# Optimization experiments

Measured on AMD Instinct MI355X. Metric: run time of the kernel, lower is better.

## Reference

```python
import jax, jax.numpy as jnp
import numpy as np

N, S, E, H = 2, 2048, 1024, 16
D = E // H  # head_dim = 64


def setup_inputs() -> dict:
    key = jax.random.key(0)
    k1, k2, k3 = jax.random.split(key, 3)
    x = jax.random.normal(k1, (N, S, E), dtype=jnp.float32)
    # Xavier-uniform-scaled weights (torch Linear layout: [out_features, in_features])
    lim_qkv = (6.0 / (E + 3 * E)) ** 0.5
    qkv_w = jax.random.uniform(k2, (3 * E, E), dtype=jnp.float32, minval=-lim_qkv, maxval=lim_qkv)
    lim_o = (6.0 / (E + E)) ** 0.5
    o_w = jax.random.uniform(k3, (E, E), dtype=jnp.float32, minval=-lim_o, maxval=lim_o)
    # causal look-ahead mask: positions where mask == 0 are excluded
    attn_mask = jnp.tril(jnp.ones((S, S), dtype=jnp.int32))
    return {"x": x, "attn_mask": attn_mask, "qkv_w": qkv_w, "o_w": o_w}


def reference(x, attn_mask, qkv_w, o_w):
    n, s, e = x.shape
    qkv = x @ qkv_w.T                              # (N, S, 3E)
    q, k, v = jnp.split(qkv, 3, axis=-1)
    # (N, S, E) -> (N, H, S, D)
    def to_heads(t):
        return t.reshape(n, s, H, D).transpose(0, 2, 1, 3)
    q, k, v = to_heads(q), to_heads(k), to_heads(v)
    scale = 1.0 / jnp.sqrt(jnp.asarray(D, dtype=x.dtype))
    logits = jnp.einsum('bhqd,bhkd->bhqk', q, k) * scale   # (N, H, S, S)
    mask = attn_mask.reshape(1, 1, s, s)                    # expand_mask: 2D -> (1,1,S,S)
    logits = jnp.where(mask == 0, -jnp.inf, logits)
    attn_weights = jax.nn.softmax(logits, axis=-1)
    values = jnp.einsum('bhqk,bhkd->bhqd', attn_weights, v)  # (N, H, S, D)
    values = values.transpose(0, 2, 1, 3).reshape(n, s, e)
    o = values @ o_w.T
    return o
```

## Files before the change

kernel.cpp:

```cpp
#include <hip/hip_runtime.h>
#include <math.h>

typedef unsigned short u16;
typedef unsigned int uint;
typedef __attribute__((ext_vector_type(8))) short bf16x8;
typedef __attribute__((ext_vector_type(8))) _Float16 half8;
typedef __attribute__((ext_vector_type(4))) float floatx4;

__device__ __forceinline__ u16 f2bf(float f) {
  union { float f; uint u; } c; c.f = f;
  return (u16)((c.u + 0x7FFFu + ((c.u >> 16) & 1u)) >> 16);
}
__device__ __forceinline__ float bf2f(u16 h) {
  union { uint u; float f; } c; c.u = ((uint)h) << 16;
  return c.f;
}
__device__ __forceinline__ u16 h2u(_Float16 h) {
  union { _Float16 h; u16 u; } c; c.h = h;
  return c.u;
}

#if __has_builtin(__builtin_amdgcn_exp2f)
#define EX2 __builtin_amdgcn_exp2f
#else
#define EX2 exp2f
#endif

__device__ __forceinline__ void gl_lds16(const u16* g, u16* l) {
  __builtin_amdgcn_global_load_lds(
      (const __attribute__((address_space(1))) uint*)g,
      (__attribute__((address_space(3))) uint*)l, 16, 0, 0);
}

__device__ __forceinline__ void store_c(u16* p, float v) { *p = f2bf(v); }
__device__ __forceinline__ void store_c(float* p, float v) { *p = v; }

#define ROR16(x, n)                                                        \
  __builtin_bit_cast(float, __builtin_amdgcn_update_dpp(                   \
      __builtin_bit_cast(int, (x)), __builtin_bit_cast(int, (x)),          \
      0x120 + (n), 0xF, 0xF, false))
__device__ __forceinline__ float rsum16(float x) {
  x += ROR16(x, 8); x += ROR16(x, 4); x += ROR16(x, 2); x += ROR16(x, 1);
  return x;
}

__global__ __launch_bounds__(256) void cvt_all(const float* __restrict__ x,
                                               const float* __restrict__ qw,
                                               const float* __restrict__ ow,
                                               u16* __restrict__ xb,
                                               u16* __restrict__ wb,
                                               u16* __restrict__ ob) {
  int bx = blockIdx.x;
  const float* src; u16* dst; int off;
  if (bx < 2048) { src = x; dst = xb; off = bx; }
  else if (bx < 3584) { src = qw; dst = wb; off = bx - 2048; }
  else { src = ow; dst = ob; off = bx - 3584; }
  int i = (off * 256 + threadIdx.x) * 8;
  float4 a = *(const float4*)(src + i);
  float4 b = *(const float4*)(src + i + 4);
  bf16x8 r;
  r[0] = (short)f2bf(a.x); r[1] = (short)f2bf(a.y);
  r[2] = (short)f2bf(a.z); r[3] = (short)f2bf(a.w);
  r[4] = (short)f2bf(b.x); r[5] = (short)f2bf(b.y);
  r[6] = (short)f2bf(b.z); r[7] = (short)f2bf(b.w);
  *(bf16x8*)(dst + i) = r;
}

__global__ __launch_bounds__(256) void vtrans(const u16* __restrict__ qkv,
                                              u16* __restrict__ vt) {
  constexpr int S = 2048, E = 1024, TE = 3072;
  __shared__ u16 tile[64 * 72];
  const int t = threadIdx.x;
  const int kv0 = blockIdx.x * 64;
  const int bh = blockIdx.y, b = bh >> 4, h = bh & 15;
  const u16* src = qkv + (size_t)b * S * TE + 2 * E + h * 64;
#pragma unroll
  for (int i = 0; i < 2; ++i) {
    int c = t + i * 256;
    int kv = c >> 3, d0 = (c & 7) * 8;
    *(bf16x8*)&tile[kv * 72 + d0] = *(const bf16x8*)&src[(size_t)(kv0 + kv) * TE + d0];
  }
  __syncthreads();
  u16* dst = vt + (size_t)bh * 64 * S + kv0;
#pragma unroll
  for (int i = 0; i < 2; ++i) {
    int c = t + i * 256;
    int d = c >> 3, k0 = (c & 7) * 8;
    bf16x8 r;
#pragma unroll
    for (int j = 0; j < 8; ++j)
      r[j] = (short)h2u((_Float16)bf2f(tile[(k0 + j) * 72 + d]));
    *(bf16x8*)&dst[(size_t)d * S + k0] = r;
  }
}

template <typename TC>
__global__ __launch_bounds__(256) void gemm_bt(const u16* __restrict__ A,
                                               const u16* __restrict__ B,
                                               TC* __restrict__ C,
                                               int K, int N) {
  __shared__ __align__(16) u16 lds_a[128 * 64];
  __shared__ __align__(16) u16 lds_b[128 * 64];
  const int t = threadIdx.x;
  const int w = t >> 6, lane = t & 63, quad = lane >> 4, lr = lane & 15;
  const int wr = w >> 1, wc = w & 1;
  const int m0 = blockIdx.y * 128, n0 = blockIdx.x * 128;

  const int srow = lane >> 3;
  const int scol = ((lane & 7) ^ srow) * 8;
  const u16* Ab = A + (size_t)(m0 + w * 32 + srow) * K + scol;
  const u16* Bb = B + (size_t)(n0 + w * 32 + srow) * K + scol;
  u16* la = lds_a + (w * 32) * 64;
  u16* lb = lds_b + (w * 32) * 64;

  floatx4 acc[4][4];
#pragma unroll
  for (int i = 0; i < 4; ++i)
#pragma unroll
    for (int j = 0; j < 4; ++j) acc[i][j] = {0.f, 0.f, 0.f, 0.f};

  for (int k0 = 0; k0 < K; k0 += 64) {
#pragma unroll
    for (int j = 0; j < 4; ++j) {
      gl_lds16(Ab + (size_t)(j * 8) * K + k0, la + j * 8 * 64);
      gl_lds16(Bb + (size_t)(j * 8) * K + k0, lb + j * 8 * 64);
    }
    __syncthreads();
#pragma unroll
    for (int kk = 0; kk < 2; ++kk) {
      bf16x8 af[4], bfr[4];
#pragma unroll
      for (int mi = 0; mi < 4; ++mi)
        af[mi] = *(const bf16x8*)&lds_a[(wr * 64 + mi * 16 + lr) * 64 +
                                        (((kk * 4 + quad) ^ (lr & 7)) * 8)];
#pragma unroll
      for (int ni = 0; ni < 4; ++ni)
        bfr[ni] = *(const bf16x8*)&lds_b[(wc * 64 + ni * 16 + lr) * 64 +
                                         (((kk * 4 + quad) ^ (lr & 7)) * 8)];
#pragma unroll
      for (int mi = 0; mi < 4; ++mi)
#pragma unroll
        for (int ni = 0; ni < 4; ++ni)
          acc[mi][ni] = __builtin_amdgcn_mfma_f32_16x16x32_bf16(
              af[mi], bfr[ni], acc[mi][ni], 0, 0, 0);
    }
    __syncthreads();
  }
#pragma unroll
  for (int mi = 0; mi < 4; ++mi)
#pragma unroll
    for (int r = 0; r < 4; ++r) {
      int m = m0 + wr * 64 + mi * 16 + quad * 4 + r;
#pragma unroll
      for (int ni = 0; ni < 4; ++ni) {
        int n = n0 + wc * 64 + ni * 16 + lr;
        store_c(&C[(size_t)m * N + n], acc[mi][ni][r]);
      }
    }
}

template <typename TC>
__global__ __launch_bounds__(256) void gemm_bt64(const u16* __restrict__ A,
                                                 const u16* __restrict__ B,
                                                 TC* __restrict__ C,
                                                 int K, int N) {
  __shared__ __align__(16) u16 lds_a[64 * 64];
  __shared__ __align__(16) u16 lds_b[128 * 64];
  const int t = threadIdx.x;
  const int w = t >> 6, lane = t & 63, quad = lane >> 4, lr = lane & 15;
  const int m0 = blockIdx.y * 64, n0 = blockIdx.x * 128;

  const int srow = lane >> 3;
  const int scol = ((lane & 7) ^ srow) * 8;
  const u16* Ab = A + (size_t)(m0 + srow) * K + scol;
  const u16* Bb = B + (size_t)(n0 + srow) * K + scol;

  floatx4 acc[4][2];
#pragma unroll
  for (int i = 0; i < 4; ++i)
#pragma unroll
    for (int j = 0; j < 2; ++j) acc[i][j] = {0.f, 0.f, 0.f, 0.f};

  for (int k0 = 0; k0 < K; k0 += 64) {
#pragma unroll
    for (int i = 0; i < 2; ++i)
      gl_lds16(Ab + (size_t)((w * 2 + i) * 8) * K + k0, &lds_a[(w * 2 + i) * 8 * 64]);
#pragma unroll
    for (int i = 0; i < 4; ++i)
      gl_lds16(Bb + (size_t)((w * 4 + i) * 8) * K + k0, &lds_b[(w * 4 + i) * 8 * 64]);
    __syncthreads();
#pragma unroll
    for (int kk = 0; kk < 2; ++kk) {
      bf16x8 af[4], bfr[2];
#pragma unroll
      for (int mi = 0; mi < 4; ++mi)
        af[mi] = *(const bf16x8*)&lds_a[(mi * 16 + lr) * 64 +
                                        (((kk * 4 + quad) ^ (lr & 7)) * 8)];
#pragma unroll
      for (int ni = 0; ni < 2; ++ni)
        bfr[ni] = *(const bf16x8*)&lds_b[(w * 32 + ni * 16 + lr) * 64 +
                                         (((kk * 4 + quad) ^ (lr & 7)) * 8)];
#pragma unroll
      for (int mi = 0; mi < 4; ++mi)
#pragma unroll
        for (int ni = 0; ni < 2; ++ni)
          acc[mi][ni] = __builtin_amdgcn_mfma_f32_16x16x32_bf16(
              af[mi], bfr[ni], acc[mi][ni], 0, 0, 0);
    }
    __syncthreads();
  }
#pragma unroll
  for (int mi = 0; mi < 4; ++mi)
#pragma unroll
    for (int r = 0; r < 4; ++r) {
      int m = m0 + mi * 16 + quad * 4 + r;
#pragma unroll
      for (int ni = 0; ni < 2; ++ni) {
        int n = n0 + w * 32 + ni * 16 + lr;
        store_c(&C[(size_t)m * N + n], acc[mi][ni][r]);
      }
    }
}

__global__ __launch_bounds__(256, 1) void attn_fwd(const u16* __restrict__ qkv,
                                                   const u16* __restrict__ vt,
                                                   u16* __restrict__ out) {
  constexpr int S = 2048, E = 1024, TE = 3072;
  constexpr float NEG = -1e30f;
  __shared__ __align__(16) u16 lds_k[2][128 * 64];
  __shared__ __align__(16) u16 lds_vt[2][64 * 128];
  __shared__ __align__(16) u16 lds_p[4][16 * 128];
  const int t = threadIdx.x;
  const int w = t >> 6, lane = t & 63, quad = lane >> 4, lr = lane & 15;
  const int lin = (int)blockIdx.x;
  const int xcd = lin & 7, j = lin >> 3;
  const int pass = j >> 5, k = j & 31;
  const int bh = xcd + 8 * (k & 3);
  const int qrank = k >> 2;
  const int qt = pass ? qrank : (15 - qrank);
  const int b = bh >> 4, h = bh & 15;
  const size_t base = (size_t)b * S * TE;
  const u16* kbase = qkv + base + E + h * 64;
  const u16* vtb = vt + (size_t)bh * 64 * S;

  const int s8 = lane >> 3;
  const int kcol = ((lane & 7) ^ s8) * 8;
  const int vrow = lane >> 4;
  u16* const pb = &lds_p[w][0];

  const int q0 = qt * 128;
  const int nkt = qt + 1;

  const float QS = 0.125f * 1.44269504f;
  bf16x8 qf[2][2];
#pragma unroll
  for (int rg = 0; rg < 2; ++rg)
#pragma unroll
    for (int kk = 0; kk < 2; ++kk) {
      bf16x8 q = *(const bf16x8*)&qkv[base +
          (size_t)(q0 + w * 32 + rg * 16 + lr) * TE + h * 64 + kk * 32 + quad * 8];
#pragma unroll
      for (int jj = 0; jj < 8; ++jj) q[jj] = (short)f2bf(bf2f((u16)q[jj]) * QS);
      qf[rg][kk] = q;
    }

  float lst[2][4];
  floatx4 oacc[2][4];
#pragma unroll
  for (int rg = 0; rg < 2; ++rg)
#pragma unroll
    for (int r = 0; r < 4; ++r) { lst[rg][r] = 0.f; }
#pragma unroll
  for (int rg = 0; rg < 2; ++rg)
#pragma unroll
    for (int di = 0; di < 4; ++di) oacc[rg][di] = {0.f, 0.f, 0.f, 0.f};

#pragma unroll
  for (int i = 0; i < 4; ++i) {
    int p0 = w * 8 + i * 32;
    int kv = ((p0 & 15) + s8) * 8 + (p0 >> 4);
    gl_lds16(kbase + (size_t)kv * TE + kcol, &lds_k[0][p0 * 64]);
  }
#pragma unroll
  for (int i = 0; i < 4; ++i) {
    int d0 = w * 4 + i * 16;
    int d = d0 + vrow;
    int cbg = ((lane & 15) ^ (d & 15)) * 8;
    gl_lds16(vtb + (size_t)d * S + cbg, &lds_vt[0][d0 * 128]);
  }

  for (int kt = 0; kt < nkt; ++kt) {
    const int bi = kt & 1;
    __syncthreads();
    if (kt + 1 < nkt) {
      const int bn = bi ^ 1;
#pragma unroll
      for (int i = 0; i < 4; ++i) {
        int p0 = w * 8 + i * 32;
        int kv = 128 * (kt + 1) + ((p0 & 15) + s8) * 8 + (p0 >> 4);
        gl_lds16(kbase + (size_t)kv * TE + kcol, &lds_k[bn][p0 * 64]);
      }
#pragma unroll
      for (int i = 0; i < 4; ++i) {
        int d0 = w * 4 + i * 16;
        int d = d0 + vrow;
        int cbg = ((lane & 15) ^ (d & 15)) * 8;
        gl_lds16(vtb + (size_t)d * S + 128 * (kt + 1) + cbg,
                 &lds_vt[bn][d0 * 128]);
      }
    }

    floatx4 st[2][8];
#pragma unroll
    for (int rg = 0; rg < 2; ++rg)
#pragma unroll
      for (int ni = 0; ni < 8; ++ni) st[rg][ni] = {-4.f, -4.f, -4.f, -4.f};
#pragma unroll
    for (int kk = 0; kk < 2; ++kk) {
      bf16x8 kb[8];
#pragma unroll
      for (int ni = 0; ni < 8; ++ni)
        kb[ni] = *(const bf16x8*)&lds_k[bi][(ni * 16 + lr) * 64 +
                                           (((kk * 4 + quad) ^ (lr & 7)) * 8)];
#pragma unroll
      for (int rg = 0; rg < 2; ++rg)
#pragma unroll
        for (int ni = 0; ni < 8; ++ni)
          st[rg][ni] = __builtin_amdgcn_mfma_f32_16x16x32_bf16(
              qf[rg][kk], kb[ni], st[rg][ni], 0, 0, 0);
    }

    half8 vb[4][4];
#pragma unroll
    for (int kk = 0; kk < 4; ++kk)
#pragma unroll
      for (int di = 0; di < 4; ++di)
        vb[kk][di] = *(const half8*)&lds_vt[bi][(di * 16 + lr) * 128 +
                                                (((kk * 4 + quad) ^ lr) << 3)];

    const bool diag = (kt == nkt - 1);
#pragma unroll
    for (int rg = 0; rg < 2; ++rg) {
#pragma unroll
      for (int r = 0; r < 4; ++r) {
        const int rw = quad * 4 + r;
        const int rloc = w * 32 + rg * 16 + rw;
        if (diag) {
#pragma unroll
          for (int ni = 0; ni < 8; ++ni)
            if (lr * 8 + ni > rloc) st[rg][ni][r] = NEG;
        }
        float pv[8];
#pragma unroll
        for (int ni = 0; ni < 8; ++ni) pv[ni] = EX2(st[rg][ni][r]);
        lst[rg][r] += ((pv[0] + pv[1]) + (pv[2] + pv[3])) +
                      ((pv[4] + pv[5]) + (pv[6] + pv[7]));
        half8 p8;
#pragma unroll
        for (int ni = 0; ni < 8; ++ni) p8[ni] = (_Float16)pv[ni];
        *(half8*)&pb[rw * 128 + (((lr + rw) & 15) << 3)] = p8;
      }
#pragma unroll
      for (int kk = 0; kk < 4; ++kk) {
        half8 pf = *(const half8*)&pb[lr * 128 +
                                      ((((kk * 4 + quad) + lr) & 15) << 3)];
#pragma unroll
        for (int di = 0; di < 4; ++di)
          oacc[rg][di] = __builtin_amdgcn_mfma_f32_16x16x32_f16(
              pf, vb[kk][di], oacc[rg][di], 0, 0, 0);
      }
    }
  }

#pragma unroll
  for (int rg = 0; rg < 2; ++rg)
#pragma unroll
    for (int r = 0; r < 4; ++r) {
      int sg = q0 + w * 32 + rg * 16 + quad * 4 + r;
      float inv_l = 1.f / rsum16(lst[rg][r]);
#pragma unroll
      for (int di = 0; di < 4; ++di)
        out[((size_t)(b * S + sg)) * E + h * 64 + di * 16 + lr] =
            f2bf(oacc[rg][di][r] * inv_l);
    }
}

extern "C" void kernel_launch(void* const* d_in, const int* in_sizes, int n_in,
                              void* d_out, int out_size, void* d_ws, size_t ws_size,
                              hipStream_t stream) {
  constexpr int NB = 2, S = 2048, E = 1024;
  constexpr int M = NB * S;
  const float* x = (const float*)d_in[0];
  const float* qkv_w = (const float*)d_in[2];
  const float* o_w = (const float*)d_in[3];
  float* out = (float*)d_out;

  u16* qkv = (u16*)d_ws;
  u16* vt = qkv + (size_t)M * 3 * E;
  u16* xb = vt + (size_t)32 * 64 * S;
  u16* attn_o = xb;
  u16* wb = xb + (size_t)M * E;
  u16* ob = wb + (size_t)3 * E * E;

  cvt_all<<<4096, 256, 0, stream>>>(x, qkv_w, o_w, xb, wb, ob);
  gemm_bt<u16><<<dim3(3 * E / 128, M / 128), 256, 0, stream>>>(xb, wb, qkv, E, 3 * E);
  vtrans<<<dim3(S / 64, NB * 16), 256, 0, stream>>>(qkv, vt);
  attn_fwd<<<512, 256, 0, stream>>>(qkv, vt, attn_o);
  gemm_bt64<float><<<dim3(E / 128, M / 64), 256, 0, stream>>>(attn_o, ob, out, E, E);
}
```

Before: 193.2 us.

## Pack both batches into one 512-thread attention block with single-buffered K/V

The attention kernel now launches 256 blocks of 512 threads, and each half-block handles the same head and query tile for one of the two batches. Each half gets its own LDS region in place of the old double buffer. K and V fragments are read into registers, and after a second barrier the next tile is loaded into the same buffer, so the loads overlap the softmax and PV work. The XCD-aware block swizzle and the heavy-first causal ordering are removed, and launch bounds change to (512, 2). The costs are an extra barrier per iteration shared by eight waves, and possible load imbalance or worse L2 locality now that the ordering is gone.

```diff
diff --git a/kernel.cpp b/kernel.cpp
--- a/kernel.cpp
+++ b/kernel.cpp
@@ -222,23 +222,23 @@
     }
 }
 
-__global__ __launch_bounds__(256, 1) void attn_fwd(const u16* __restrict__ qkv,
+__global__ __launch_bounds__(512, 2) void attn_fwd(const u16* __restrict__ qkv,
                                                    const u16* __restrict__ vt,
                                                    u16* __restrict__ out) {
   constexpr int S = 2048, E = 1024, TE = 3072;
   constexpr float NEG = -1e30f;
   __shared__ __align__(16) u16 lds_k[2][128 * 64];
   __shared__ __align__(16) u16 lds_vt[2][64 * 128];
-  __shared__ __align__(16) u16 lds_p[4][16 * 128];
+  __shared__ __align__(16) u16 lds_p[2][4][16 * 128];
   const int t = threadIdx.x;
-  const int w = t >> 6, lane = t & 63, quad = lane >> 4, lr = lane & 15;
-  const int lin = (int)blockIdx.x;
-  const int xcd = lin & 7, j = lin >> 3;
-  const int pass = j >> 5, k = j & 31;
-  const int bh = xcd + 8 * (k & 3);
-  const int qrank = k >> 2;
-  const int qt = pass ? qrank : (15 - qrank);
-  const int b = bh >> 4, h = bh & 15;
+  const int wv = t >> 6;
+  const int u = wv >> 2;
+  const int w = wv & 3;
+  const int lane = t & 63, quad = lane >> 4, lr = lane & 15;
+  const int bx = (int)blockIdx.x;
+  const int h = bx & 15, qt = bx >> 4;
+  const int b = u;
+  const int bh = b * 16 + h;
   const size_t base = (size_t)b * S * TE;
   const u16* kbase = qkv + base + E + h * 64;
   const u16* vtb = vt + (size_t)bh * 64 * S;
@@ -246,7 +246,9 @@
   const int s8 = lane >> 3;
   const int kcol = ((lane & 7) ^ s8) * 8;
   const int vrow = lane >> 4;
-  u16* const pb = &lds_p[w][0];
+  u16* const pb = &lds_p[u][w][0];
+  u16* const lk = &lds_k[u][0];
+  u16* const lv = &lds_vt[u][0];
 
   const int q0 = qt * 128;
   const int nkt = qt + 1;
@@ -279,64 +281,64 @@
   for (int i = 0; i < 4; ++i) {
     int p0 = w * 8 + i * 32;
     int kv = ((p0 & 15) + s8) * 8 + (p0 >> 4);
-    gl_lds16(kbase + (size_t)kv * TE + kcol, &lds_k[0][p0 * 64]);
+    gl_lds16(kbase + (size_t)kv * TE + kcol, &lk[p0 * 64]);
   }
 #pragma unroll
   for (int i = 0; i < 4; ++i) {
     int d0 = w * 4 + i * 16;
     int d = d0 + vrow;
     int cbg = ((lane & 15) ^ (d & 15)) * 8;
-    gl_lds16(vtb + (size_t)d * S + cbg, &lds_vt[0][d0 * 128]);
+    gl_lds16(vtb + (size_t)d * S + cbg, &lv[d0 * 128]);
   }
 
   for (int kt = 0; kt < nkt; ++kt) {
-    const int bi = kt & 1;
-    __syncthreads();
+    __syncthreads();
+
+    floatx4 st[2][8];
+#pragma unroll
+    for (int rg = 0; rg < 2; ++rg)
+#pragma unroll
+      for (int ni = 0; ni < 8; ++ni) st[rg][ni] = {-4.f, -4.f, -4.f, -4.f};
+#pragma unroll
+    for (int kk = 0; kk < 2; ++kk) {
+      bf16x8 kb[8];
+#pragma unroll
+      for (int ni = 0; ni < 8; ++ni)
+        kb[ni] = *(const bf16x8*)&lk[(ni * 16 + lr) * 64 +
+                                     (((kk * 4 + quad) ^ (lr & 7)) * 8)];
+#pragma unroll
+      for (int rg = 0; rg < 2; ++rg)
+#pragma unroll
+        for (int ni = 0; ni < 8; ++ni)
+          st[rg][ni] = __builtin_amdgcn_mfma_f32_16x16x32_bf16(
+              qf[rg][kk], kb[ni], st[rg][ni], 0, 0, 0);
+    }
+
+    half8 vb[4][4];
+#pragma unroll
+    for (int kk = 0; kk < 4; ++kk)
+#pragma unroll
+      for (int di = 0; di < 4; ++di)
+        vb[kk][di] = *(const half8*)&lv[(di * 16 + lr) * 128 +
+                                        (((kk * 4 + quad) ^ lr) << 3)];
+
+    __syncthreads();
+
     if (kt + 1 < nkt) {
-      const int bn = bi ^ 1;
 #pragma unroll
       for (int i = 0; i < 4; ++i) {
         int p0 = w * 8 + i * 32;
         int kv = 128 * (kt + 1) + ((p0 & 15) + s8) * 8 + (p0 >> 4);
-        gl_lds16(kbase + (size_t)kv * TE + kcol, &lds_k[bn][p0 * 64]);
+        gl_lds16(kbase + (size_t)kv * TE + kcol, &lk[p0 * 64]);
       }
 #pragma unroll
       for (int i = 0; i < 4; ++i) {
         int d0 = w * 4 + i * 16;
         int d = d0 + vrow;
         int cbg = ((lane & 15) ^ (d & 15)) * 8;
-        gl_lds16(vtb + (size_t)d * S + 128 * (kt + 1) + cbg,
-                 &lds_vt[bn][d0 * 128]);
-      }
-    }
-
-    floatx4 st[2][8];
-#pragma unroll
-    for (int rg = 0; rg < 2; ++rg)
-#pragma unroll
-      for (int ni = 0; ni < 8; ++ni) st[rg][ni] = {-4.f, -4.f, -4.f, -4.f};
-#pragma unroll
-    for (int kk = 0; kk < 2; ++kk) {
-      bf16x8 kb[8];
-#pragma unroll
-      for (int ni = 0; ni < 8; ++ni)
-        kb[ni] = *(const bf16x8*)&lds_k[bi][(ni * 16 + lr) * 64 +
-                                           (((kk * 4 + quad) ^ (lr & 7)) * 8)];
-#pragma unroll
-      for (int rg = 0; rg < 2; ++rg)
-#pragma unroll
-        for (int ni = 0; ni < 8; ++ni)
-          st[rg][ni] = __builtin_amdgcn_mfma_f32_16x16x32_bf16(
-              qf[rg][kk], kb[ni], st[rg][ni], 0, 0, 0);
-    }
-
-    half8 vb[4][4];
-#pragma unroll
-    for (int kk = 0; kk < 4; ++kk)
-#pragma unroll
-      for (int di = 0; di < 4; ++di)
-        vb[kk][di] = *(const half8*)&lds_vt[bi][(di * 16 + lr) * 128 +
-                                                (((kk * 4 + quad) ^ lr) << 3)];
+        gl_lds16(vtb + (size_t)d * S + 128 * (kt + 1) + cbg, &lv[d0 * 128]);
+      }
+    }
 
     const bool diag = (kt == nkt - 1);
 #pragma unroll
@@ -405,6 +407,6 @@
   cvt_all<<<4096, 256, 0, stream>>>(x, qkv_w, o_w, xb, wb, ob);
   gemm_bt<u16><<<dim3(3 * E / 128, M / 128), 256, 0, stream>>>(xb, wb, qkv, E, 3 * E);
   vtrans<<<dim3(S / 64, NB * 16), 256, 0, stream>>>(qkv, vt);
-  attn_fwd<<<512, 256, 0, stream>>>(qkv, vt, attn_o);
+  attn_fwd<<<256, 512, 0, stream>>>(qkv, vt, attn_o);
   gemm_bt64<float><<<dim3(E / 128, M / 64), 256, 0, stream>>>(attn_o, ob, out, E, E);
 }
```

Result: faster. 188.9 us (-2.3%).
